# Performance work log

Hardware: AMD Instinct MI355X
Metric: run time of the kernel (lower is better)

## Reference

```python
import jax, jax.numpy as jnp
import numpy as np

N, E, G = 100000, 800000, 1
DV, DE, DU, H = 64, 32, 32, 128

def _w(key, shape):
    return jax.random.normal(key, shape, dtype=jnp.float32) * 0.05

def setup_inputs() -> dict:
    key = jax.random.key(0)
    ks = jax.random.split(key, 16)
    inp = {
        "node_attr": jax.random.normal(ks[0], (N, DV), dtype=jnp.float32),
        "edges": jax.random.randint(ks[1], (2, E), 0, N, dtype=jnp.int64 if jax.config.jax_enable_x64 else jnp.int32),
        "edge_attr": jax.random.normal(ks[2], (E, DE), dtype=jnp.float32),
        "u": jax.random.normal(ks[3], (G, DU), dtype=jnp.float32),
        "node_idx": jnp.zeros((N,), dtype=jnp.int32),
        "edge_idx": jnp.zeros((E,), dtype=jnp.int32),
        # edge MLP: concat(src, dst, edge_attr, u) -> H -> H
        "W1e": _w(ks[4], (2 * DV + DE + DU, H)), "b1e": jnp.zeros((H,), jnp.float32),
        "W2e": _w(ks[5], (H, H)), "b2e": jnp.zeros((H,), jnp.float32),
        # node MLP: concat(node_attr, aggregated_edges, u) -> H -> H
        "W1n": _w(ks[6], (DV + H + DU, H)), "b1n": jnp.zeros((H,), jnp.float32),
        "W2n": _w(ks[7], (H, H)), "b2n": jnp.zeros((H,), jnp.float32),
        # global MLP: concat(node_mean, edge_mean, u) -> H -> H
        "W1g": _w(ks[8], (H + H + DU, H)), "b1g": jnp.zeros((H,), jnp.float32),
        "W2g": _w(ks[9], (H, H)), "b2g": jnp.zeros((H,), jnp.float32),
    }
    return inp

def _mlp(x, W1, b1, W2, b2):
    return jax.nn.relu(x @ W1 + b1) @ W2 + b2

def _seg_mean(x, seg, num):
    s = jax.ops.segment_sum(x, seg, num_segments=num)
    c = jax.ops.segment_sum(jnp.ones((x.shape[0], 1), x.dtype), seg, num_segments=num)
    return s / jnp.maximum(c, 1.0)

def reference(node_attr, edges, edge_attr, u, node_idx, edge_idx,
              W1e, b1e, W2e, b2e, W1n, b1n, W2n, b2n, W1g, b1g, W2g, b2g):
    row, col = edges[0], edges[1]
    # edge model: gather endpoint features, concat with edge/global attrs
    e_in = jnp.concatenate([node_attr[row], node_attr[col], edge_attr, u[edge_idx]], axis=-1)
    e = _mlp(e_in, W1e, b1e, W2e, b2e)                        # [E, H]
    # node model: scatter-add incoming edge messages onto receivers (col)
    agg = jax.ops.segment_sum(e, col, num_segments=node_attr.shape[0])  # [N, H]
    v_in = jnp.concatenate([node_attr, agg, u[node_idx]], axis=-1)
    v = _mlp(v_in, W1n, b1n, W2n, b2n)                        # [N, H]
    # global model: per-graph mean pooling of nodes and edges
    nv = _seg_mean(v, node_idx, u.shape[0])                   # [G, H]
    ne = _seg_mean(e, edge_idx, u.shape[0])                   # [G, H]
    g_in = jnp.concatenate([nv, ne, u], axis=-1)
    g = _mlp(g_in, W1g, b1g, W2g, b2g)                        # [G, H]
    return v, e, g
```

## Files before the change

kernel.cpp:

```cpp
#include <hip/hip_runtime.h>

#define N_NODES 100000
#define N_EDGES 800000
#define DV 64
#define DE 32
#define DU 32
#define H 128

typedef short bf16x8 __attribute__((ext_vector_type(8)));
typedef unsigned short u16;
typedef u16 u16x8 __attribute__((ext_vector_type(8)));
typedef float f32x4 __attribute__((ext_vector_type(4)));

#define OFF_ESUM 0
#define OFF_VSUM 8192
#define OFF_PART 16384
#define OFF_WBUF 18432
#define OFF_DEG  190464
#define OFF_OFFS 590464
#define OFF_BUCK 990464

#define W1ET_OFF 0
#define W2ET_OFF 24576
#define W1NT_OFF 40960
#define W2NT_OFF 69632
#define WBUF_ELEMS 86016

#define NPART 391

__device__ inline u16 f2bf(float x) {
  union { float f; unsigned u; } c; c.f = x;
  unsigned r = c.u + 0x7FFFu + ((c.u >> 16) & 1u);
  return (u16)(r >> 16);
}

__global__ void prep_weights(const float* __restrict__ W1e, const float* __restrict__ W2e,
                             const float* __restrict__ W1n, const float* __restrict__ W2n,
                             u16* __restrict__ wbuf) {
  int i = blockIdx.x * blockDim.x + threadIdx.x;
  if (i < 24576) {
    int j = i / 192, k = i - j * 192;
    wbuf[W1ET_OFF + i] = f2bf(W1e[k * H + j]);
  } else if (i < 40960) {
    int t = i - 24576; int j = t >> 7, k = t & 127;
    wbuf[i] = f2bf(W2e[k * H + j]);
  } else if (i < 69632) {
    int t = i - 40960; int j = t / 224, k = t - j * 224;
    wbuf[i] = f2bf(W1n[k * H + j]);
  } else if (i < WBUF_ELEMS) {
    int t = i - 69632; int j = t >> 7, k = t & 127;
    wbuf[i] = f2bf(W2n[k * H + j]);
  }
}

__global__ void degree_kernel(const int* __restrict__ edges, int* __restrict__ deg) {
  int i = blockIdx.x * 256 + threadIdx.x;
  if (i < N_EDGES) atomicAdd(&deg[edges[N_EDGES + i]], 1);
}

__global__ void scan_part(const int* __restrict__ deg, int* __restrict__ part) {
  int i = blockIdx.x * 256 + threadIdx.x;
  int v = (i < N_NODES) ? deg[i] : 0;
#pragma unroll
  for (int m = 1; m < 64; m <<= 1) v += __shfl_xor(v, m);
  __shared__ int s[4];
  if ((threadIdx.x & 63) == 0) s[threadIdx.x >> 6] = v;
  __syncthreads();
  if (threadIdx.x == 0) part[blockIdx.x] = s[0] + s[1] + s[2] + s[3];
}

__global__ void scan_top(int* __restrict__ part) {
  __shared__ int s[512];
  int t = threadIdx.x;
  s[t] = (t < NPART) ? part[t] : 0;
  __syncthreads();
  for (int d = 1; d < 512; d <<= 1) {
    int v = (t >= d) ? s[t - d] : 0;
    __syncthreads();
    s[t] += v;
    __syncthreads();
  }
  if (t < NPART) part[t] = (t == 0) ? 0 : s[t - 1];
}

__global__ void scan_down(const int* __restrict__ part, int* __restrict__ deg_cursor,
                          int* __restrict__ offsets) {
  __shared__ int s[256];
  int b = blockIdx.x, t = threadIdx.x;
  int i = b * 256 + t;
  int v = (i < N_NODES) ? deg_cursor[i] : 0;
  s[t] = v;
  __syncthreads();
  for (int d = 1; d < 256; d <<= 1) {
    int u = (t >= d) ? s[t - d] : 0;
    __syncthreads();
    s[t] += u;
    __syncthreads();
  }
  int excl = s[t] - v + part[b];
  if (i < N_NODES) { offsets[i] = excl; deg_cursor[i] = excl; }
}

__global__ void fill_kernel(const int* __restrict__ edges, int* __restrict__ cursor,
                            int* __restrict__ bucket) {
  int i = blockIdx.x * 256 + threadIdx.x;
  if (i < N_EDGES) {
    int d = edges[N_EDGES + i];
    int pos = atomicAdd(&cursor[d], 1);
    bucket[pos] = i;
  }
}

__global__ __launch_bounds__(256, 3) void edge_kernel(
    const float* __restrict__ node_attr, const int* __restrict__ edges,
    const float* __restrict__ edge_attr, const float* __restrict__ uattr,
    const int* __restrict__ edge_idx, const u16* __restrict__ wbuf,
    const float* __restrict__ b1, const float* __restrict__ b2,
    float* __restrict__ e_out, float* __restrict__ esum_p)
{
  __shared__ __align__(16) char smem[43008];
  u16 (*X)[200]   = (u16(*)[200])smem;
  u16 (*Hs)[136]  = (u16(*)[136])(smem + 25600);
  float (*OT)[132] = (float(*)[132])smem;
  __shared__ int sSrc[64], sDst[64], sEidx[64];

  const int tid = threadIdx.x;
  const int wave = tid >> 6, lane = tid & 63;
  const int l15 = lane & 15, lg = lane >> 4;
  const long e0 = (long)blockIdx.x * 64;
  const int wc = wave * 32;

  if (tid < 64)        sSrc[tid]        = edges[e0 + tid];
  else if (tid < 128)  sDst[tid - 64]   = edges[(long)N_EDGES + e0 + (tid - 64)];
  else if (tid < 192)  sEidx[tid - 128] = edge_idx[e0 + (tid - 128)];

  bf16x8 w1[6][2], w2[4][2];
  {
    const u16* w1t = wbuf + W1ET_OFF;
    const u16* w2t = wbuf + W2ET_OFF;
#pragma unroll
    for (int cf = 0; cf < 2; ++cf) {
      const u16* p1 = w1t + (wc + cf * 16 + l15) * 192 + lg * 8;
#pragma unroll
      for (int ks = 0; ks < 6; ++ks) w1[ks][cf] = *(const bf16x8*)(p1 + ks * 32);
      const u16* p2 = w2t + (wc + cf * 16 + l15) * 128 + lg * 8;
#pragma unroll
      for (int ks = 0; ks < 4; ++ks) w2[ks][cf] = *(const bf16x8*)(p2 + ks * 32);
    }
  }

  __syncthreads();

#pragma unroll
  for (int it = 0; it < 6; ++it) {
    int ch = tid + it * 256;
    int r = ch / 24, seg = ch - r * 24;
    int col = seg * 8;
    const float* src;
    if (col < 64)        src = node_attr + (long)sSrc[r] * DV + col;
    else if (col < 128)  src = node_attr + (long)sDst[r] * DV + (col - 64);
    else if (col < 160)  src = edge_attr + (e0 + r) * DE + (col - 128);
    else                 src = uattr + (long)sEidx[r] * DU + (col - 160);
    float4 f0 = *(const float4*)src;
    float4 f1 = *(const float4*)(src + 4);
    u16x8 p;
    p[0] = f2bf(f0.x); p[1] = f2bf(f0.y); p[2] = f2bf(f0.z); p[3] = f2bf(f0.w);
    p[4] = f2bf(f1.x); p[5] = f2bf(f1.y); p[6] = f2bf(f1.z); p[7] = f2bf(f1.w);
    *(u16x8*)&X[r][col] = p;
  }

  __syncthreads();

  f32x4 acc[4][2];
#pragma unroll
  for (int rf = 0; rf < 4; ++rf)
#pragma unroll
    for (int cf = 0; cf < 2; ++cf)
#pragma unroll
      for (int j = 0; j < 4; ++j) acc[rf][cf][j] = 0.f;

#pragma unroll
  for (int ks = 0; ks < 6; ++ks) {
#pragma unroll
    for (int rf = 0; rf < 4; ++rf) {
      bf16x8 a = *(const bf16x8*)&X[rf * 16 + l15][ks * 32 + lg * 8];
      acc[rf][0] = __builtin_amdgcn_mfma_f32_16x16x32_bf16(a, w1[ks][0], acc[rf][0], 0, 0, 0);
      acc[rf][1] = __builtin_amdgcn_mfma_f32_16x16x32_bf16(a, w1[ks][1], acc[rf][1], 0, 0, 0);
    }
  }

  float bias1[2] = { b1[wc + l15], b1[wc + 16 + l15] };
#pragma unroll
  for (int rf = 0; rf < 4; ++rf)
#pragma unroll
    for (int cf = 0; cf < 2; ++cf)
#pragma unroll
      for (int j = 0; j < 4; ++j) {
        float hv = acc[rf][cf][j] + bias1[cf];
        hv = hv > 0.f ? hv : 0.f;
        Hs[rf * 16 + lg * 4 + j][wc + cf * 16 + l15] = f2bf(hv);
      }

  __syncthreads();

#pragma unroll
  for (int rf = 0; rf < 4; ++rf)
#pragma unroll
    for (int cf = 0; cf < 2; ++cf)
#pragma unroll
      for (int j = 0; j < 4; ++j) acc[rf][cf][j] = 0.f;

#pragma unroll
  for (int ks = 0; ks < 4; ++ks) {
#pragma unroll
    for (int rf = 0; rf < 4; ++rf) {
      bf16x8 a = *(const bf16x8*)&Hs[rf * 16 + l15][ks * 32 + lg * 8];
      acc[rf][0] = __builtin_amdgcn_mfma_f32_16x16x32_bf16(a, w2[ks][0], acc[rf][0], 0, 0, 0);
      acc[rf][1] = __builtin_amdgcn_mfma_f32_16x16x32_bf16(a, w2[ks][1], acc[rf][1], 0, 0, 0);
    }
  }

  __syncthreads();

  float bias2[2] = { b2[wc + l15], b2[wc + 16 + l15] };
  float es0 = 0.f, es1 = 0.f;
#pragma unroll
  for (int rf = 0; rf < 4; ++rf) {
#pragma unroll
    for (int cf = 0; cf < 2; ++cf) {
#pragma unroll
      for (int j = 0; j < 4; ++j) {
        float v = acc[rf][cf][j] + bias2[cf];
        OT[rf * 16 + lg * 4 + j][wc + cf * 16 + l15] = v;
        if (cf == 0) es0 += v; else es1 += v;
      }
    }
  }

  __syncthreads();

#pragma unroll
  for (int i = 0; i < 8; ++i) {
    int ch = tid + i * 256;
    int r = ch >> 5, c4 = ch & 31;
    float4 f = *(const float4*)&OT[r][c4 * 4];
    *(float4*)(e_out + (e0 + r) * H + c4 * 4) = f;
  }

#pragma unroll
  for (int m = 16; m < 64; m <<= 1) { es0 += __shfl_xor(es0, m); es1 += __shfl_xor(es1, m); }
  if (lane < 16) {
    atomicAdd(&esum_p[(wc + lane) * 16], es0);
    atomicAdd(&esum_p[(wc + 16 + lane) * 16], es1);
  }
}

__global__ __launch_bounds__(256, 3) void node_kernel(
    const float* __restrict__ node_attr, const float* __restrict__ uattr,
    const int* __restrict__ node_idx, const u16* __restrict__ wbuf,
    const float* __restrict__ b1, const float* __restrict__ b2,
    const float* __restrict__ e_out, const int* __restrict__ offsets,
    const int* __restrict__ cursor, const int* __restrict__ bucket,
    float* __restrict__ v_out, float* __restrict__ vsum_p)
{
  __shared__ __align__(16) u16 X[64][232];
  __shared__ __align__(16) u16 Hs[64][136];

  const int tid = threadIdx.x;
  const int wave = tid >> 6, lane = tid & 63;
  const int l15 = lane & 15, lg = lane >> 4;
  const long n0 = (long)blockIdx.x * 64;
  const int wc = wave * 32;

  {
    int gr = tid >> 2, gq = tid & 3;
    long gn = n0 + gr;
    float a[32];
#pragma unroll
    for (int k = 0; k < 32; ++k) a[k] = 0.f;
    if (gn < N_NODES) {
      int s = offsets[gn], e = cursor[gn];
      for (int i = s; i < e; ++i) {
        int eid = bucket[i];
        const float* p = e_out + (long)eid * H + gq * 32;
#pragma unroll
        for (int k = 0; k < 8; ++k) {
          float4 f = *(const float4*)(p + k * 4);
          a[k * 4 + 0] += f.x; a[k * 4 + 1] += f.y;
          a[k * 4 + 2] += f.z; a[k * 4 + 3] += f.w;
        }
      }
    }
#pragma unroll
    for (int k = 0; k < 4; ++k) {
      u16x8 pk;
#pragma unroll
      for (int j = 0; j < 8; ++j) pk[j] = f2bf(a[k * 8 + j]);
      *(u16x8*)&X[gr][64 + gq * 32 + k * 8] = pk;
    }
  }

#pragma unroll
  for (int it = 0; it < 3; ++it) {
    int ch = tid + it * 256;
    int r = ch / 12, seg = ch - r * 12;
    long n = n0 + r; if (n >= N_NODES) n = N_NODES - 1;
    const float* src;
    int col;
    if (seg < 8) { col = seg * 8;            src = node_attr + n * DV + col; }
    else         { col = 192 + (seg - 8) * 8; src = uattr + (long)node_idx[n] * DU + (seg - 8) * 8; }
    float4 f0 = *(const float4*)src;
    float4 f1 = *(const float4*)(src + 4);
    u16x8 p;
    p[0] = f2bf(f0.x); p[1] = f2bf(f0.y); p[2] = f2bf(f0.z); p[3] = f2bf(f0.w);
    p[4] = f2bf(f1.x); p[5] = f2bf(f1.y); p[6] = f2bf(f1.z); p[7] = f2bf(f1.w);
    *(u16x8*)&X[r][col] = p;
  }

  bf16x8 w1[7][2], w2[4][2];
  {
    const u16* w1t = wbuf + W1NT_OFF;
    const u16* w2t = wbuf + W2NT_OFF;
#pragma unroll
    for (int cf = 0; cf < 2; ++cf) {
      const u16* p1 = w1t + (wc + cf * 16 + l15) * 224 + lg * 8;
#pragma unroll
      for (int ks = 0; ks < 7; ++ks) w1[ks][cf] = *(const bf16x8*)(p1 + ks * 32);
      const u16* p2 = w2t + (wc + cf * 16 + l15) * 128 + lg * 8;
#pragma unroll
      for (int ks = 0; ks < 4; ++ks) w2[ks][cf] = *(const bf16x8*)(p2 + ks * 32);
    }
  }

  __syncthreads();

  f32x4 acc[4][2];
#pragma unroll
  for (int rf = 0; rf < 4; ++rf)
#pragma unroll
    for (int cf = 0; cf < 2; ++cf)
#pragma unroll
      for (int j = 0; j < 4; ++j) acc[rf][cf][j] = 0.f;

#pragma unroll
  for (int ks = 0; ks < 7; ++ks) {
#pragma unroll
    for (int rf = 0; rf < 4; ++rf) {
      bf16x8 a = *(const bf16x8*)&X[rf * 16 + l15][ks * 32 + lg * 8];
      acc[rf][0] = __builtin_amdgcn_mfma_f32_16x16x32_bf16(a, w1[ks][0], acc[rf][0], 0, 0, 0);
      acc[rf][1] = __builtin_amdgcn_mfma_f32_16x16x32_bf16(a, w1[ks][1], acc[rf][1], 0, 0, 0);
    }
  }

  float bias1[2] = { b1[wc + l15], b1[wc + 16 + l15] };
#pragma unroll
  for (int rf = 0; rf < 4; ++rf)
#pragma unroll
    for (int cf = 0; cf < 2; ++cf)
#pragma unroll
      for (int j = 0; j < 4; ++j) {
        float hv = acc[rf][cf][j] + bias1[cf];
        hv = hv > 0.f ? hv : 0.f;
        Hs[rf * 16 + lg * 4 + j][wc + cf * 16 + l15] = f2bf(hv);
      }

  __syncthreads();

#pragma unroll
  for (int rf = 0; rf < 4; ++rf)
#pragma unroll
    for (int cf = 0; cf < 2; ++cf)
#pragma unroll
      for (int j = 0; j < 4; ++j) acc[rf][cf][j] = 0.f;

#pragma unroll
  for (int ks = 0; ks < 4; ++ks) {
#pragma unroll
    for (int rf = 0; rf < 4; ++rf) {
      bf16x8 a = *(const bf16x8*)&Hs[rf * 16 + l15][ks * 32 + lg * 8];
      acc[rf][0] = __builtin_amdgcn_mfma_f32_16x16x32_bf16(a, w2[ks][0], acc[rf][0], 0, 0, 0);
      acc[rf][1] = __builtin_amdgcn_mfma_f32_16x16x32_bf16(a, w2[ks][1], acc[rf][1], 0, 0, 0);
    }
  }

  float bias2[2] = { b2[wc + l15], b2[wc + 16 + l15] };
  float vs0 = 0.f, vs1 = 0.f;
#pragma unroll
  for (int rf = 0; rf < 4; ++rf) {
#pragma unroll
    for (int cf = 0; cf < 2; ++cf) {
      int colg = wc + cf * 16 + l15;
#pragma unroll
      for (int j = 0; j < 4; ++j) {
        int r = rf * 16 + lg * 4 + j;
        long n = n0 + r;
        if (n < N_NODES) {
          float v = acc[rf][cf][j] + bias2[cf];
          v_out[n * H + colg] = v;
          if (cf == 0) vs0 += v; else vs1 += v;
        }
      }
    }
  }
#pragma unroll
  for (int m = 16; m < 64; m <<= 1) { vs0 += __shfl_xor(vs0, m); vs1 += __shfl_xor(vs1, m); }
  if (lane < 16) {
    atomicAdd(&vsum_p[(wc + lane) * 16], vs0);
    atomicAdd(&vsum_p[(wc + 16 + lane) * 16], vs1);
  }
}

__global__ void global_kernel(const float* __restrict__ uattr,
    const float* __restrict__ W1g, const float* __restrict__ b1g,
    const float* __restrict__ W2g, const float* __restrict__ b2g,
    const float* __restrict__ esum_p, const float* __restrict__ vsum_p,
    float* __restrict__ g_out)
{
  __shared__ float gin[288];
  __shared__ float hbuf[128];
  int t = threadIdx.x;
  gin[t]       = vsum_p[t * 16] * (1.f / (float)N_NODES);
  gin[128 + t] = esum_p[t * 16] * (1.f / (float)N_EDGES);
  if (t < 32) gin[256 + t] = uattr[t];
  __syncthreads();
  float a = b1g[t];
  for (int k = 0; k < 288; ++k) a += gin[k] * W1g[k * H + t];
  hbuf[t] = fmaxf(a, 0.f);
  __syncthreads();
  float b = b2g[t];
  for (int k = 0; k < 128; ++k) b += hbuf[k] * W2g[k * H + t];
  g_out[t] = b;
}

extern "C" void kernel_launch(void* const* d_in, const int* in_sizes, int n_in,
                              void* d_out, int out_size, void* d_ws, size_t ws_size,
                              hipStream_t stream) {
  const float* node_attr = (const float*)d_in[0];
  const int*   edges     = (const int*)d_in[1];
  const float* edge_attr = (const float*)d_in[2];
  const float* uattr     = (const float*)d_in[3];
  const int*   node_idx  = (const int*)d_in[4];
  const int*   edge_idx  = (const int*)d_in[5];
  const float* W1e = (const float*)d_in[6];  const float* b1e = (const float*)d_in[7];
  const float* W2e = (const float*)d_in[8];  const float* b2e = (const float*)d_in[9];
  const float* W1n = (const float*)d_in[10]; const float* b1n = (const float*)d_in[11];
  const float* W2n = (const float*)d_in[12]; const float* b2n = (const float*)d_in[13];
  const float* W1g = (const float*)d_in[14]; const float* b1g = (const float*)d_in[15];
  const float* W2g = (const float*)d_in[16]; const float* b2g = (const float*)d_in[17];

  float* out   = (float*)d_out;
  float* v_out = out;
  float* e_out = out + (long)N_NODES * H;
  float* g_out = out + (long)N_NODES * H + (long)N_EDGES * H;

  char* ws = (char*)d_ws;
  float* esum_p = (float*)(ws + OFF_ESUM);
  float* vsum_p = (float*)(ws + OFF_VSUM);
  int*   part   = (int*)(ws + OFF_PART);
  u16*   wbuf   = (u16*)(ws + OFF_WBUF);
  int*   deg    = (int*)(ws + OFF_DEG);
  int*   offs   = (int*)(ws + OFF_OFFS);
  int*   buck   = (int*)(ws + OFF_BUCK);

  hipMemsetAsync(ws, 0, 16384, stream);
  hipMemsetAsync(deg, 0, N_NODES * sizeof(int), stream);

  prep_weights<<<WBUF_ELEMS / 256, 256, 0, stream>>>(W1e, W2e, W1n, W2n, wbuf);
  degree_kernel<<<(N_EDGES + 255) / 256, 256, 0, stream>>>(edges, deg);
  scan_part<<<NPART, 256, 0, stream>>>(deg, part);
  scan_top<<<1, 512, 0, stream>>>(part);
  scan_down<<<NPART, 256, 0, stream>>>(part, deg, offs);
  fill_kernel<<<(N_EDGES + 255) / 256, 256, 0, stream>>>(edges, deg, buck);

  edge_kernel<<<N_EDGES / 64, 256, 0, stream>>>(node_attr, edges, edge_attr, uattr,
                                                edge_idx, wbuf, b1e, b2e,
                                                e_out, esum_p);
  node_kernel<<<(N_NODES + 63) / 64, 256, 0, stream>>>(node_attr, uattr, node_idx,
                                                       wbuf, b1n, b2n,
                                                       e_out, offs, deg, buck,
                                                       v_out, vsum_p);
  global_kernel<<<1, 128, 0, stream>>>(uattr, W1g, b1g, W2g, b2g, esum_p, vsum_p, g_out);
}
```

Before: 619.5 us.

## Make edge kernel persistent with software-pipelined gather prefetch; unroll node aggregation

The edge kernel becomes persistent with a fixed grid of 512 blocks. Each block loops over tiles and prefetches the next tile's gathered inputs into registers, and the tile after that's indices into double-buffered shared memory, so gather latency overlaps the MFMA work. Weights and biases are loaded once per block instead of once per tile. Occupancy drops from 3 to 2 blocks per CU, and plain __syncthreads is replaced by explicit lgkmcnt-wait barriers. The node aggregation loop processes two edges per iteration to raise memory-level parallelism.

Result: no change. 609.9 us (-1.5%).

```diff
diff --git a/kernel.cpp b/kernel.cpp
--- a/kernel.cpp
+++ b/kernel.cpp
@@ -6,6 +6,9 @@
 #define DE 32
 #define DU 32
 #define H 128
+
+#define NTILES 12500
+#define EGRID  512
 
 typedef short bf16x8 __attribute__((ext_vector_type(8)));
 typedef unsigned short u16;
@@ -32,6 +35,12 @@
   union { float f; unsigned u; } c; c.f = x;
   unsigned r = c.u + 0x7FFFu + ((c.u >> 16) & 1u);
   return (u16)(r >> 16);
+}
+
+__device__ inline void bar_lgkm() {
+  asm volatile("s_waitcnt lgkmcnt(0)" ::: "memory");
+  __builtin_amdgcn_sched_barrier(0);
+  __builtin_amdgcn_s_barrier();
 }
 
 __global__ void prep_weights(const float* __restrict__ W1e, const float* __restrict__ W2e,
@@ -111,7 +120,7 @@
   }
 }
 
-__global__ __launch_bounds__(256, 3) void edge_kernel(
+__global__ __launch_bounds__(256, 2) void edge_kernel(
     const float* __restrict__ node_attr, const int* __restrict__ edges,
     const float* __restrict__ edge_attr, const float* __restrict__ uattr,
     const int* __restrict__ edge_idx, const u16* __restrict__ wbuf,
@@ -119,20 +128,25 @@
     float* __restrict__ e_out, float* __restrict__ esum_p)
 {
   __shared__ __align__(16) char smem[43008];
-  u16 (*X)[200]   = (u16(*)[200])smem;
-  u16 (*Hs)[136]  = (u16(*)[136])(smem + 25600);
+  u16 (*X)[200]    = (u16(*)[200])smem;
+  u16 (*Hs)[136]   = (u16(*)[136])(smem + 25600);
   float (*OT)[132] = (float(*)[132])smem;
-  __shared__ int sSrc[64], sDst[64], sEidx[64];
+  __shared__ int sIdx[2][3][64];
 
   const int tid = threadIdx.x;
-  const int wave = tid >> 6, lane = tid & 63;
+  const int lane = tid & 63;
+  const int wave = tid >> 6;
   const int l15 = lane & 15, lg = lane >> 4;
-  const long e0 = (long)blockIdx.x * 64;
   const int wc = wave * 32;
-
-  if (tid < 64)        sSrc[tid]        = edges[e0 + tid];
-  else if (tid < 128)  sDst[tid - 64]   = edges[(long)N_EDGES + e0 + (tid - 64)];
-  else if (tid < 192)  sEidx[tid - 128] = edge_idx[e0 + (tid - 128)];
+  const int bid = blockIdx.x;
+
+  int r_[6], c_[6];
+#pragma unroll
+  for (int it = 0; it < 6; ++it) {
+    int ch = tid + it * 256;
+    r_[it] = ch / 24;
+    c_[it] = (ch - r_[it] * 24) * 8;
+  }
 
   bf16x8 w1[6][2], w2[4][2];
   {
@@ -148,103 +162,151 @@
       for (int ks = 0; ks < 4; ++ks) w2[ks][cf] = *(const bf16x8*)(p2 + ks * 32);
     }
   }
-
-  __syncthreads();
-
-#pragma unroll
-  for (int it = 0; it < 6; ++it) {
-    int ch = tid + it * 256;
-    int r = ch / 24, seg = ch - r * 24;
-    int col = seg * 8;
-    const float* src;
-    if (col < 64)        src = node_attr + (long)sSrc[r] * DV + col;
-    else if (col < 128)  src = node_attr + (long)sDst[r] * DV + (col - 64);
-    else if (col < 160)  src = edge_attr + (e0 + r) * DE + (col - 128);
-    else                 src = uattr + (long)sEidx[r] * DU + (col - 160);
-    float4 f0 = *(const float4*)src;
-    float4 f1 = *(const float4*)(src + 4);
-    u16x8 p;
-    p[0] = f2bf(f0.x); p[1] = f2bf(f0.y); p[2] = f2bf(f0.z); p[3] = f2bf(f0.w);
-    p[4] = f2bf(f1.x); p[5] = f2bf(f1.y); p[6] = f2bf(f1.z); p[7] = f2bf(f1.w);
-    *(u16x8*)&X[r][col] = p;
-  }
-
-  __syncthreads();
-
-  f32x4 acc[4][2];
-#pragma unroll
-  for (int rf = 0; rf < 4; ++rf)
-#pragma unroll
-    for (int cf = 0; cf < 2; ++cf)
-#pragma unroll
-      for (int j = 0; j < 4; ++j) acc[rf][cf][j] = 0.f;
-
-#pragma unroll
-  for (int ks = 0; ks < 6; ++ks) {
+  float bias1[2] = { b1[wc + l15], b1[wc + 16 + l15] };
+  float bias2[2] = { b2[wc + l15], b2[wc + 16 + l15] };
+
+  const int nt = (NTILES - 1 - bid) / EGRID + 1;
+
+  float4 G[12];
+  int gi = 0;
+
+  auto IDX_LOAD = [&](long t) {
+    if (tid < 64)        gi = edges[t * 64 + tid];
+    else if (tid < 128)  gi = edges[(long)N_EDGES + t * 64 + (tid - 64)];
+    else if (tid < 192)  gi = edge_idx[t * 64 + (tid - 128)];
+  };
+  auto IDX_WRITE = [&](int buf) {
+    if (tid < 64)        sIdx[buf][0][tid] = gi;
+    else if (tid < 128)  sIdx[buf][1][tid - 64] = gi;
+    else if (tid < 192)  sIdx[buf][2][tid - 128] = gi;
+  };
+  auto ISSUE = [&](long t, int buf) {
+    long e0c = t * 64;
+#pragma unroll
+    for (int it = 0; it < 6; ++it) {
+      int r = r_[it], col = c_[it];
+      const float* src;
+      if (col < 64)       src = node_attr + (long)sIdx[buf][0][r] * DV + col;
+      else if (col < 128) src = node_attr + (long)sIdx[buf][1][r] * DV + (col - 64);
+      else if (col < 160) src = edge_attr + (e0c + r) * DE + (col - 128);
+      else                src = uattr + (long)sIdx[buf][2][r] * DU + (col - 160);
+      G[it * 2]     = *(const float4*)src;
+      G[it * 2 + 1] = *(const float4*)(src + 4);
+    }
+  };
+  auto WRITE_X = [&]() {
+#pragma unroll
+    for (int it = 0; it < 6; ++it) {
+      float4 f0 = G[it * 2], f1 = G[it * 2 + 1];
+      u16x8 p;
+      p[0] = f2bf(f0.x); p[1] = f2bf(f0.y); p[2] = f2bf(f0.z); p[3] = f2bf(f0.w);
+      p[4] = f2bf(f1.x); p[5] = f2bf(f1.y); p[6] = f2bf(f1.z); p[7] = f2bf(f1.w);
+      *(u16x8*)&X[r_[it]][c_[it]] = p;
+    }
+  };
+
+  IDX_LOAD((long)bid);
+  IDX_WRITE(0);
+  bar_lgkm();
+  ISSUE((long)bid, 0);
+  if (nt > 1) IDX_LOAD((long)bid + EGRID);
+  WRITE_X();
+  if (nt > 1) IDX_WRITE(1);
+  bar_lgkm();
+  if (nt > 1) ISSUE((long)bid + EGRID, 1);
+
+  float es0 = 0.f, es1 = 0.f;
+
+  for (int ti = 0; ti < nt; ++ti) {
+    long t = (long)bid + (long)ti * EGRID;
+    const bool hasN1 = (ti + 1 < nt);
+    const bool hasN2 = (ti + 2 < nt);
+
+    if (hasN2) IDX_LOAD(t + 2 * EGRID);
+
+    f32x4 acc[4][2];
+#pragma unroll
+    for (int rf = 0; rf < 4; ++rf)
+#pragma unroll
+      for (int cf = 0; cf < 2; ++cf)
+#pragma unroll
+        for (int j = 0; j < 4; ++j) acc[rf][cf][j] = 0.f;
+
+#pragma unroll
+    for (int ks = 0; ks < 6; ++ks) {
+#pragma unroll
+      for (int rf = 0; rf < 4; ++rf) {
+        bf16x8 a = *(const bf16x8*)&X[rf * 16 + l15][ks * 32 + lg * 8];
+        acc[rf][0] = __builtin_amdgcn_mfma_f32_16x16x32_bf16(a, w1[ks][0], acc[rf][0], 0, 0, 0);
+        acc[rf][1] = __builtin_amdgcn_mfma_f32_16x16x32_bf16(a, w1[ks][1], acc[rf][1], 0, 0, 0);
+      }
+    }
+
+#pragma unroll
+    for (int rf = 0; rf < 4; ++rf)
+#pragma unroll
+      for (int cf = 0; cf < 2; ++cf)
+#pragma unroll
+        for (int j = 0; j < 4; ++j) {
+          float hv = acc[rf][cf][j] + bias1[cf];
+          hv = hv > 0.f ? hv : 0.f;
+          Hs[rf * 16 + lg * 4 + j][wc + cf * 16 + l15] = f2bf(hv);
+        }
+
+    bar_lgkm();
+
+#pragma unroll
+    for (int rf = 0; rf < 4; ++rf)
+#pragma unroll
+      for (int cf = 0; cf < 2; ++cf)
+#pragma unroll
+        for (int j = 0; j < 4; ++j) acc[rf][cf][j] = 0.f;
+
+#pragma unroll
+    for (int ks = 0; ks < 4; ++ks) {
+#pragma unroll
+      for (int rf = 0; rf < 4; ++rf) {
+        bf16x8 a = *(const bf16x8*)&Hs[rf * 16 + l15][ks * 32 + lg * 8];
+        acc[rf][0] = __builtin_amdgcn_mfma_f32_16x16x32_bf16(a, w2[ks][0], acc[rf][0], 0, 0, 0);
+        acc[rf][1] = __builtin_amdgcn_mfma_f32_16x16x32_bf16(a, w2[ks][1], acc[rf][1], 0, 0, 0);
+      }
+    }
+
+    bar_lgkm();
+
 #pragma unroll
     for (int rf = 0; rf < 4; ++rf) {
-      bf16x8 a = *(const bf16x8*)&X[rf * 16 + l15][ks * 32 + lg * 8];
-      acc[rf][0] = __builtin_amdgcn_mfma_f32_16x16x32_bf16(a, w1[ks][0], acc[rf][0], 0, 0, 0);
-      acc[rf][1] = __builtin_amdgcn_mfma_f32_16x16x32_bf16(a, w1[ks][1], acc[rf][1], 0, 0, 0);
-    }
-  }
-
-  float bias1[2] = { b1[wc + l15], b1[wc + 16 + l15] };
-#pragma unroll
-  for (int rf = 0; rf < 4; ++rf)
-#pragma unroll
-    for (int cf = 0; cf < 2; ++cf)
-#pragma unroll
-      for (int j = 0; j < 4; ++j) {
-        float hv = acc[rf][cf][j] + bias1[cf];
-        hv = hv > 0.f ? hv : 0.f;
-        Hs[rf * 16 + lg * 4 + j][wc + cf * 16 + l15] = f2bf(hv);
-      }
-
-  __syncthreads();
-
-#pragma unroll
-  for (int rf = 0; rf < 4; ++rf)
-#pragma unroll
-    for (int cf = 0; cf < 2; ++cf)
-#pragma unroll
-      for (int j = 0; j < 4; ++j) acc[rf][cf][j] = 0.f;
-
-#pragma unroll
-  for (int ks = 0; ks < 4; ++ks) {
-#pragma unroll
-    for (int rf = 0; rf < 4; ++rf) {
-      bf16x8 a = *(const bf16x8*)&Hs[rf * 16 + l15][ks * 32 + lg * 8];
-      acc[rf][0] = __builtin_amdgcn_mfma_f32_16x16x32_bf16(a, w2[ks][0], acc[rf][0], 0, 0, 0);
-      acc[rf][1] = __builtin_amdgcn_mfma_f32_16x16x32_bf16(a, w2[ks][1], acc[rf][1], 0, 0, 0);
-    }
-  }
-
-  __syncthreads();
-
-  float bias2[2] = { b2[wc + l15], b2[wc + 16 + l15] };
-  float es0 = 0.f, es1 = 0.f;
-#pragma unroll
-  for (int rf = 0; rf < 4; ++rf) {
-#pragma unroll
-    for (int cf = 0; cf < 2; ++cf) {
-#pragma unroll
-      for (int j = 0; j < 4; ++j) {
-        float v = acc[rf][cf][j] + bias2[cf];
-        OT[rf * 16 + lg * 4 + j][wc + cf * 16 + l15] = v;
-        if (cf == 0) es0 += v; else es1 += v;
-      }
-    }
-  }
-
-  __syncthreads();
-
-#pragma unroll
-  for (int i = 0; i < 8; ++i) {
-    int ch = tid + i * 256;
-    int r = ch >> 5, c4 = ch & 31;
-    float4 f = *(const float4*)&OT[r][c4 * 4];
-    *(float4*)(e_out + (e0 + r) * H + c4 * 4) = f;
+#pragma unroll
+      for (int cf = 0; cf < 2; ++cf) {
+#pragma unroll
+        for (int j = 0; j < 4; ++j) {
+          float v = acc[rf][cf][j] + bias2[cf];
+          OT[rf * 16 + lg * 4 + j][wc + cf * 16 + l15] = v;
+          if (cf == 0) es0 += v; else es1 += v;
+        }
+      }
+    }
+
+    bar_lgkm();
+
+    {
+      long e0c = t * 64;
+#pragma unroll
+      for (int i = 0; i < 8; ++i) {
+        int ch = tid + i * 256;
+        int r = ch >> 5, c4 = ch & 31;
+        float4 f = *(const float4*)&OT[r][c4 * 4];
+        *(float4*)(e_out + (e0c + r) * H + c4 * 4) = f;
+      }
+    }
+
+    bar_lgkm();
+
+    if (hasN1) WRITE_X();
+    if (hasN2) IDX_WRITE(ti & 1);
+    bar_lgkm();
+
+    if (hasN2) ISSUE(t + 2 * EGRID, ti & 1);
   }
 
 #pragma unroll
@@ -280,12 +342,30 @@
     for (int k = 0; k < 32; ++k) a[k] = 0.f;
     if (gn < N_NODES) {
       int s = offsets[gn], e = cursor[gn];
-      for (int i = s; i < e; ++i) {
-        int eid = bucket[i];
-        const float* p = e_out + (long)eid * H + gq * 32;
+      int i = s;
+      for (; i + 2 <= e; i += 2) {
+        int e0 = bucket[i], e1 = bucket[i + 1];
+        const float* p0 = e_out + (long)e0 * H + gq * 32;
+        const float* p1 = e_out + (long)e1 * H + gq * 32;
+        float4 f0[8], f1[8];
+#pragma unroll
+        for (int k = 0; k < 8; ++k) f0[k] = *(const float4*)(p0 + k * 4);
+#pragma unroll
+        for (int k = 0; k < 8; ++k) f1[k] = *(const float4*)(p1 + k * 4);
 #pragma unroll
         for (int k = 0; k < 8; ++k) {
-          float4 f = *(const float4*)(p + k * 4);
+          a[k * 4 + 0] += f0[k].x + f1[k].x;
+          a[k * 4 + 1] += f0[k].y + f1[k].y;
+          a[k * 4 + 2] += f0[k].z + f1[k].z;
+          a[k * 4 + 3] += f0[k].w + f1[k].w;
+        }
+      }
+      if (i < e) {
+        int e0 = bucket[i];
+        const float* p0 = e_out + (long)e0 * H + gq * 32;
+#pragma unroll
+        for (int k = 0; k < 8; ++k) {
+          float4 f = *(const float4*)(p0 + k * 4);
           a[k * 4 + 0] += f.x; a[k * 4 + 1] += f.y;
           a[k * 4 + 2] += f.z; a[k * 4 + 3] += f.w;
         }
@@ -307,7 +387,7 @@
     long n = n0 + r; if (n >= N_NODES) n = N_NODES - 1;
     const float* src;
     int col;
-    if (seg < 8) { col = seg * 8;            src = node_attr + n * DV + col; }
+    if (seg < 8) { col = seg * 8;             src = node_attr + n * DV + col; }
     else         { col = 192 + (seg - 8) * 8; src = uattr + (long)node_idx[n] * DU + (seg - 8) * 8; }
     float4 f0 = *(const float4*)src;
     float4 f1 = *(const float4*)(src + 4);
@@ -472,9 +552,9 @@
   scan_down<<<NPART, 256, 0, stream>>>(part, deg, offs);
   fill_kernel<<<(N_EDGES + 255) / 256, 256, 0, stream>>>(edges, deg, buck);
 
-  edge_kernel<<<N_EDGES / 64, 256, 0, stream>>>(node_attr, edges, edge_attr, uattr,
-                                                edge_idx, wbuf, b1e, b2e,
-                                                e_out, esum_p);
+  edge_kernel<<<EGRID, 256, 0, stream>>>(node_attr, edges, edge_attr, uattr,
+                                         edge_idx, wbuf, b1e, b2e,
+                                         e_out, esum_p);
   node_kernel<<<(N_NODES + 63) / 64, 256, 0, stream>>>(node_attr, uattr, node_idx,
                                                        wbuf, b1n, b2n,
                                                        e_out, offs, deg, buck,
```

## Process edges in destination-sorted order and fuse segment-sum aggregation into edge kernel

Applied to the files above, without the earlier changes.

The fill pass now writes permuted src, dst and graph-index arrays, so the edge kernel processes edges grouped by receiver node, with XCD-aware tile remapping. In the edge epilogue, half the threads reduce runs of equal destinations in shared memory and write partial sums straight into a zeroed v_out buffer. Interior runs use plain stores and only the boundary runs use atomics. The node kernel then reads agg from that buffer instead of re-gathering all edge outputs through the bucket list. The cost is scattered e_out writes and edge_attr gathers by original edge id, plus an extra memset and larger fill writes.

Result: no change. 630.1 us (+1.7%).

```diff
diff --git a/kernel.cpp b/kernel.cpp
--- a/kernel.cpp
+++ b/kernel.cpp
@@ -7,18 +7,23 @@
 #define DU 32
 #define H 128
 
+#define NTILES 12500
+
 typedef short bf16x8 __attribute__((ext_vector_type(8)));
 typedef unsigned short u16;
 typedef u16 u16x8 __attribute__((ext_vector_type(8)));
 typedef float f32x4 __attribute__((ext_vector_type(4)));
 
-#define OFF_ESUM 0
-#define OFF_VSUM 8192
-#define OFF_PART 16384
-#define OFF_WBUF 18432
-#define OFF_DEG  190464
-#define OFF_OFFS 590464
-#define OFF_BUCK 990464
+#define OFF_ESUM  0
+#define OFF_VSUM  8192
+#define OFF_PART  16384
+#define OFF_WBUF  18432
+#define OFF_DEG   190464
+#define OFF_OFFS  590464
+#define OFF_BUCK  990464
+#define OFF_DSTP  4190464
+#define OFF_SRCP  7390464
+#define OFF_EIDXP 10590464
 
 #define W1ET_OFF 0
 #define W2ET_OFF 24576
@@ -101,38 +106,51 @@
   if (i < N_NODES) { offsets[i] = excl; deg_cursor[i] = excl; }
 }
 
-__global__ void fill_kernel(const int* __restrict__ edges, int* __restrict__ cursor,
-                            int* __restrict__ bucket) {
+__global__ void fill_kernel(const int* __restrict__ edges, const int* __restrict__ edge_idx,
+                            int* __restrict__ cursor, int* __restrict__ bucket,
+                            int* __restrict__ dstP, int* __restrict__ srcP,
+                            int* __restrict__ eidxP) {
   int i = blockIdx.x * 256 + threadIdx.x;
   if (i < N_EDGES) {
+    int s = edges[i];
     int d = edges[N_EDGES + i];
     int pos = atomicAdd(&cursor[d], 1);
     bucket[pos] = i;
+    dstP[pos] = d;
+    srcP[pos] = s;
+    eidxP[pos] = edge_idx[i];
   }
 }
 
 __global__ __launch_bounds__(256, 3) void edge_kernel(
-    const float* __restrict__ node_attr, const int* __restrict__ edges,
-    const float* __restrict__ edge_attr, const float* __restrict__ uattr,
-    const int* __restrict__ edge_idx, const u16* __restrict__ wbuf,
+    const float* __restrict__ node_attr, const float* __restrict__ edge_attr,
+    const float* __restrict__ uattr, const u16* __restrict__ wbuf,
     const float* __restrict__ b1, const float* __restrict__ b2,
-    float* __restrict__ e_out, float* __restrict__ esum_p)
+    const int* __restrict__ bucket, const int* __restrict__ dstP,
+    const int* __restrict__ srcP, const int* __restrict__ eidxP,
+    float* __restrict__ e_out, float* __restrict__ agg, float* __restrict__ esum_p)
 {
   __shared__ __align__(16) char smem[43008];
-  u16 (*X)[200]   = (u16(*)[200])smem;
-  u16 (*Hs)[136]  = (u16(*)[136])(smem + 25600);
+  u16 (*X)[200]    = (u16(*)[200])smem;
+  u16 (*Hs)[136]   = (u16(*)[136])(smem + 25600);
   float (*OT)[132] = (float(*)[132])smem;
-  __shared__ int sSrc[64], sDst[64], sEidx[64];
+  __shared__ int sSrc[64], sDst[64], sEid[64], sEidx[64];
 
   const int tid = threadIdx.x;
   const int wave = tid >> 6, lane = tid & 63;
   const int l15 = lane & 15, lg = lane >> 4;
-  const long e0 = (long)blockIdx.x * 64;
   const int wc = wave * 32;
 
-  if (tid < 64)        sSrc[tid]        = edges[e0 + tid];
-  else if (tid < 128)  sDst[tid - 64]   = edges[(long)N_EDGES + e0 + (tid - 64)];
-  else if (tid < 192)  sEidx[tid - 128] = edge_idx[e0 + (tid - 128)];
+  int b = blockIdx.x;
+  const int q = NTILES / 8, r8 = NTILES % 8;
+  int xcd = b & 7, pos = b >> 3;
+  long t = (xcd < r8 ? xcd * (q + 1) : r8 * (q + 1) + (xcd - r8) * q) + pos;
+  const long i0 = t * 64;
+
+  if (tid < 64)        sSrc[tid]        = srcP[i0 + tid];
+  else if (tid < 128)  sDst[tid - 64]   = dstP[i0 + (tid - 64)];
+  else if (tid < 192)  sEid[tid - 128]  = bucket[i0 + (tid - 128)];
+  else                 sEidx[tid - 192] = eidxP[i0 + (tid - 192)];
 
   bf16x8 w1[6][2], w2[4][2];
   {
@@ -159,7 +177,7 @@
     const float* src;
     if (col < 64)        src = node_attr + (long)sSrc[r] * DV + col;
     else if (col < 128)  src = node_attr + (long)sDst[r] * DV + (col - 64);
-    else if (col < 160)  src = edge_attr + (e0 + r) * DE + (col - 128);
+    else if (col < 160)  src = edge_attr + (long)sEid[r] * DE + (col - 128);
     else                 src = uattr + (long)sEidx[r] * DU + (col - 160);
     float4 f0 = *(const float4*)src;
     float4 f1 = *(const float4*)(src + 4);
@@ -239,12 +257,29 @@
 
   __syncthreads();
 
-#pragma unroll
-  for (int i = 0; i < 8; ++i) {
-    int ch = tid + i * 256;
-    int r = ch >> 5, c4 = ch & 31;
-    float4 f = *(const float4*)&OT[r][c4 * 4];
-    *(float4*)(e_out + (e0 + r) * H + c4 * 4) = f;
+  if (tid < 128) {
+    const int c = tid;
+    float sum = OT[0][c];
+    int runStart = 0;
+    int dprev = sDst[0];
+    for (int r = 1; r < 64; ++r) {
+      int d = sDst[r];
+      if (d != dprev) {
+        if (runStart == 0) atomicAdd(&agg[(long)dprev * H + c], sum);
+        else               agg[(long)dprev * H + c] = sum;
+        runStart = r; sum = 0.f; dprev = d;
+      }
+      sum += OT[r][c];
+    }
+    atomicAdd(&agg[(long)dprev * H + c], sum);
+  } else {
+#pragma unroll
+    for (int i = 0; i < 16; ++i) {
+      int ch = (tid - 128) + i * 128;
+      int r = ch >> 5, c4 = ch & 31;
+      float4 f = *(const float4*)&OT[r][c4 * 4];
+      *(float4*)(e_out + (long)sEid[r] * H + c4 * 4) = f;
+    }
   }
 
 #pragma unroll
@@ -259,9 +294,7 @@
     const float* __restrict__ node_attr, const float* __restrict__ uattr,
     const int* __restrict__ node_idx, const u16* __restrict__ wbuf,
     const float* __restrict__ b1, const float* __restrict__ b2,
-    const float* __restrict__ e_out, const int* __restrict__ offsets,
-    const int* __restrict__ cursor, const int* __restrict__ bucket,
-    float* __restrict__ v_out, float* __restrict__ vsum_p)
+    float* __restrict__ vio, float* __restrict__ vsum_p)
 {
   __shared__ __align__(16) u16 X[64][232];
   __shared__ __align__(16) u16 Hs[64][136];
@@ -272,43 +305,16 @@
   const long n0 = (long)blockIdx.x * 64;
   const int wc = wave * 32;
 
-  {
-    int gr = tid >> 2, gq = tid & 3;
-    long gn = n0 + gr;
-    float a[32];
-#pragma unroll
-    for (int k = 0; k < 32; ++k) a[k] = 0.f;
-    if (gn < N_NODES) {
-      int s = offsets[gn], e = cursor[gn];
-      for (int i = s; i < e; ++i) {
-        int eid = bucket[i];
-        const float* p = e_out + (long)eid * H + gq * 32;
-#pragma unroll
-        for (int k = 0; k < 8; ++k) {
-          float4 f = *(const float4*)(p + k * 4);
-          a[k * 4 + 0] += f.x; a[k * 4 + 1] += f.y;
-          a[k * 4 + 2] += f.z; a[k * 4 + 3] += f.w;
-        }
-      }
-    }
-#pragma unroll
-    for (int k = 0; k < 4; ++k) {
-      u16x8 pk;
-#pragma unroll
-      for (int j = 0; j < 8; ++j) pk[j] = f2bf(a[k * 8 + j]);
-      *(u16x8*)&X[gr][64 + gq * 32 + k * 8] = pk;
-    }
-  }
-
-#pragma unroll
-  for (int it = 0; it < 3; ++it) {
+#pragma unroll
+  for (int it = 0; it < 7; ++it) {
     int ch = tid + it * 256;
-    int r = ch / 12, seg = ch - r * 12;
+    int r = ch / 28, seg = ch - r * 28;
+    int col = seg * 8;
     long n = n0 + r; if (n >= N_NODES) n = N_NODES - 1;
     const float* src;
-    int col;
-    if (seg < 8) { col = seg * 8;            src = node_attr + n * DV + col; }
-    else         { col = 192 + (seg - 8) * 8; src = uattr + (long)node_idx[n] * DU + (seg - 8) * 8; }
+    if (col < 64)        src = node_attr + n * DV + col;
+    else if (col < 192)  src = vio + n * H + (col - 64);
+    else                 src = uattr + (long)node_idx[n] * DU + (col - 192);
     float4 f0 = *(const float4*)src;
     float4 f1 = *(const float4*)(src + 4);
     u16x8 p;
@@ -396,7 +402,7 @@
         long n = n0 + r;
         if (n < N_NODES) {
           float v = acc[rf][cf][j] + bias2[cf];
-          v_out[n * H + colg] = v;
+          vio[n * H + colg] = v;
           if (cf == 0) vs0 += v; else vs1 += v;
         }
       }
@@ -461,23 +467,26 @@
   int*   deg    = (int*)(ws + OFF_DEG);
   int*   offs   = (int*)(ws + OFF_OFFS);
   int*   buck   = (int*)(ws + OFF_BUCK);
+  int*   dstP   = (int*)(ws + OFF_DSTP);
+  int*   srcP   = (int*)(ws + OFF_SRCP);
+  int*   eidxP  = (int*)(ws + OFF_EIDXP);
 
   hipMemsetAsync(ws, 0, 16384, stream);
   hipMemsetAsync(deg, 0, N_NODES * sizeof(int), stream);
+  hipMemsetAsync(v_out, 0, (size_t)N_NODES * H * sizeof(float), stream);
 
   prep_weights<<<WBUF_ELEMS / 256, 256, 0, stream>>>(W1e, W2e, W1n, W2n, wbuf);
   degree_kernel<<<(N_EDGES + 255) / 256, 256, 0, stream>>>(edges, deg);
   scan_part<<<NPART, 256, 0, stream>>>(deg, part);
   scan_top<<<1, 512, 0, stream>>>(part);
   scan_down<<<NPART, 256, 0, stream>>>(part, deg, offs);
-  fill_kernel<<<(N_EDGES + 255) / 256, 256, 0, stream>>>(edges, deg, buck);
-
-  edge_kernel<<<N_EDGES / 64, 256, 0, stream>>>(node_attr, edges, edge_attr, uattr,
-                                                edge_idx, wbuf, b1e, b2e,
-                                                e_out, esum_p);
+  fill_kernel<<<(N_EDGES + 255) / 256, 256, 0, stream>>>(edges, edge_idx, deg,
+                                                         buck, dstP, srcP, eidxP);
+
+  edge_kernel<<<NTILES, 256, 0, stream>>>(node_attr, edge_attr, uattr, wbuf,
+                                          b1e, b2e, buck, dstP, srcP, eidxP,
+                                          e_out, v_out, esum_p);
   node_kernel<<<(N_NODES + 63) / 64, 256, 0, stream>>>(node_attr, uattr, node_idx,
-                                                       wbuf, b1n, b2n,
-                                                       e_out, offs, deg, buck,
-                                                       v_out, vsum_p);
+                                                       wbuf, b1n, b2n, v_out, vsum_p);
   global_kernel<<<1, 128, 0, stream>>>(uattr, W1g, b1g, W2g, b2g, esum_p, vsum_p, g_out);
 }
```
